# Performance work log

Hardware: AMD Instinct MI355X
Metric: run time of the kernel (lower is better)

## Reference

```python
import jax, jax.numpy as jnp
import numpy as np

H = 8  # num_attention_heads
DH = 64  # attention_head_size
D = H * DH  # hidden_size = 512
LN_EPS = 1e-6


def setup_inputs() -> dict:
    key = jax.random.key(0)
    ks = jax.random.split(key, 12)
    B, L = 32, 196
    s = 1.0 / np.sqrt(D)
    return {
        "query_states": jax.random.normal(ks[0], (B, L, D), jnp.float32),
        "key_states": jax.random.normal(ks[1], (B, L, D), jnp.float32),
        "value_states": jax.random.normal(ks[2], (B, L, D), jnp.float32),
        "Wq": jax.random.normal(ks[3], (D, D), jnp.float32) * s,
        "bq": jnp.zeros((D,), jnp.float32),
        "Wk": jax.random.normal(ks[4], (D, D), jnp.float32) * s,
        "bk": jnp.zeros((D,), jnp.float32),
        "Wv": jax.random.normal(ks[5], (D, D), jnp.float32) * s,
        "bv": jnp.zeros((D,), jnp.float32),
        "ln_gamma": jnp.ones((D,), jnp.float32),
        "ln_beta": jnp.zeros((D,), jnp.float32),
        "logit_scale": jnp.ones((), jnp.float32),
    }


def _heads(x):
    # (B, L, D) -> (B, H, L, DH)
    B, L, _ = x.shape
    return x.reshape(B, L, H, DH).transpose(0, 2, 1, 3)


def reference(query_states, key_states, value_states, Wq, bq, Wk, bk, Wv, bv,
              ln_gamma, ln_beta, logit_scale):
    B, L, _ = query_states.shape
    q = _heads(query_states @ Wq.T + bq)  # (B,H,L,DH)
    k = _heads(key_states @ Wk.T + bk)
    v = _heads(value_states @ Wv.T + bv)

    # cross-batch retrieval: sum over heads and head_dim -> (a,b,l,m)
    retrieve = jnp.einsum('ahld,bhmd->ablm', q, k)
    mask_sum = jnp.float32(L)  # mask is all-ones (B, L)
    t2v = retrieve.max(axis=-1).sum(axis=2) / mask_sum  # (a,b)
    v2t = retrieve.max(axis=-2).sum(axis=2) / mask_sum  # (a,b)
    retrieve_logits = jnp.exp(logit_scale) * (t2v + v2t) / 2.0

    # self-attention (dropout is identity in eval)
    scores = jnp.einsum('bhld,bhmd->bhlm', q, k) / jnp.sqrt(jnp.float32(DH))
    probs = jax.nn.softmax(scores, axis=-1)  # (B,H,L,L)
    ctx = jnp.einsum('bhlm,bhmd->bhld', probs, v)
    ctx = ctx.transpose(0, 2, 1, 3).reshape(B, L, D)
    ctx = ctx + query_states

    mu = ctx.mean(axis=-1, keepdims=True)
    var = ((ctx - mu) ** 2).mean(axis=-1, keepdims=True)
    ctx = (ctx - mu) / jnp.sqrt(var + LN_EPS) * ln_gamma + ln_beta

    return ctx, retrieve_logits, probs.mean(axis=1)
```

## Files before the change

kernel.cpp:

```cpp
#include <hip/hip_runtime.h>
#include <hip/hip_bf16.h>

#define BB 32
#define LL 196
#define DD 512
#define HH 8
#define DHH 64
#define BL (BB*LL)
#define PVK 224
#define PSTR 236

typedef __bf16 bf16x8 __attribute__((ext_vector_type(8)));
typedef float f32x4 __attribute__((ext_vector_type(4)));

#define MFMA16(a,b,c) __builtin_amdgcn_mfma_f32_16x16x32_bf16((a),(b),(c),0,0,0)

#define GLOAD_LDS16(g, l) __builtin_amdgcn_global_load_lds( \
    (const __attribute__((address_space(1))) void*)(g), \
    (__attribute__((address_space(3))) void*)(l), 16, 0, 0)

static __device__ __forceinline__ bf16x8 pack8(float4 v0, float4 v1) {
  bf16x8 o;
  o[0] = (__bf16)v0.x; o[1] = (__bf16)v0.y; o[2] = (__bf16)v0.z; o[3] = (__bf16)v0.w;
  o[4] = (__bf16)v1.x; o[5] = (__bf16)v1.y; o[6] = (__bf16)v1.z; o[7] = (__bf16)v1.w;
  return o;
}

static __device__ __forceinline__ unsigned fkey(float f) {
  unsigned u = __float_as_uint(f);
  return u ^ ((unsigned)((int)u >> 31) | 0x80000000u);
}
static __device__ __forceinline__ float unkey(unsigned k) {
  unsigned u = (k & 0x80000000u) ? (k ^ 0x80000000u) : ~k;
  return __uint_as_float(u);
}

#define STAGE_PAIR(SA, SB, abase, bbase) do { \
  const __bf16* aB_ = (abase); const __bf16* bB_ = (bbase); \
  _Pragma("unroll") \
  for (int c_ = 0; c_ < 4; ++c_) { \
    const int p_ = c_ * 256 + tid; \
    GLOAD_LDS16(aB_ + (size_t)(p_ >> 3) * DD + swoff, &SA[p_ * 8]); \
  } \
  _Pragma("unroll") \
  for (int c_ = 0; c_ < 4; ++c_) { \
    const int p_ = c_ * 256 + tid; \
    GLOAD_LDS16(bB_ + (size_t)(p_ >> 3) * DD + swoff, &SB[p_ * 8]); \
  } \
} while (0)

#define COMPUTE_TILE(SA, SB) do { \
  _Pragma("unroll") \
  for (int kc_ = 0; kc_ < 2; ++kc_) { \
    const int q_ = (((kc_ * 4 + (lane >> 4)) ^ (lane & 7)) << 3); \
    bf16x8 af_[4], bf_[4]; \
    _Pragma("unroll") \
    for (int mt_ = 0; mt_ < 4; ++mt_) \
      af_[mt_] = *(const bf16x8*)&SA[(wr + mt_ * 16 + (lane & 15)) * 64 + q_]; \
    _Pragma("unroll") \
    for (int nt_ = 0; nt_ < 4; ++nt_) \
      bf_[nt_] = *(const bf16x8*)&SB[(wc + nt_ * 16 + (lane & 15)) * 64 + q_]; \
    _Pragma("unroll") \
    for (int mt_ = 0; mt_ < 4; ++mt_) \
      _Pragma("unroll") \
      for (int nt_ = 0; nt_ < 4; ++nt_) \
        acc[mt_][nt_] = MFMA16(af_[mt_], bf_[nt_], acc[mt_][nt_]); \
  } \
} while (0)

__global__ __launch_bounds__(256) void cvt_kernel(
    const float* __restrict__ x0, const float* __restrict__ x1, const float* __restrict__ x2,
    const float* __restrict__ w0, const float* __restrict__ w1, const float* __restrict__ w2,
    __bf16* __restrict__ xb, __bf16* __restrict__ wb)
{
  const int z = blockIdx.y;
  const float* src; __bf16* dst; size_t i;
  if (blockIdx.x < 1568) {
    src = (z == 0) ? x0 : (z == 1) ? x1 : x2;
    dst = xb + (size_t)z * 3211264;
    i = (size_t)blockIdx.x * 256 + threadIdx.x;
  } else {
    src = (z == 0) ? w0 : (z == 1) ? w1 : w2;
    dst = wb + (size_t)z * 262144;
    i = (size_t)(blockIdx.x - 1568) * 256 + threadIdx.x;
  }
  const float4* s = (const float4*)(src + i * 8);
  float4 a = s[0], b = s[1];
  *(bf16x8*)(dst + i * 8) = pack8(a, b);
}

__global__ __launch_bounds__(256) void proj_gemm_kernel(
    const __bf16* __restrict__ xb, const __bf16* __restrict__ wb,
    const float* __restrict__ bq, const float* __restrict__ bk, const float* __restrict__ bv,
    __bf16* __restrict__ qp, __bf16* __restrict__ kp, __bf16* __restrict__ vp)
{
  __shared__ __bf16 sA[128 * 64];
  __shared__ __bf16 sB[128 * 64];

  const int z = blockIdx.z;
  const __bf16* A = xb + (size_t)z * 3211264;
  const __bf16* B = wb + (size_t)z * 262144;
  const float* bias = (z == 0) ? bq : (z == 1) ? bk : bv;
  __bf16* out = (z == 0) ? qp : (z == 1) ? kp : vp;

  const int tid = threadIdx.x;
  const int w = tid >> 6, lane = tid & 63;
  const int wr = (w >> 1) * 64, wc = (w & 1) * 64;
  const int bm = blockIdx.x * 128, bn = blockIdx.y * 128;
  const int swoff = ((tid & 7) ^ ((tid >> 3) & 7)) << 3;

  const __bf16* aP = A + (size_t)bm * DD;
  const __bf16* bP = B + (size_t)bn * DD;

  f32x4 acc[4][4] = {};

  #pragma unroll
  for (int kt = 0; kt < 8; ++kt) {
    STAGE_PAIR(sA, sB, aP + kt * 64, bP + kt * 64);
    __syncthreads();
    COMPUTE_TILE(sA, sB);
    __syncthreads();
  }

  #pragma unroll
  for (int mt = 0; mt < 4; ++mt)
    #pragma unroll
    for (int nt = 0; nt < 4; ++nt)
      #pragma unroll
      for (int rr = 0; rr < 4; ++rr) {
        const int row = bm + wr + mt * 16 + (lane >> 4) * 4 + rr;
        const int col = bn + wc + nt * 16 + (lane & 15);
        out[(size_t)row * DD + col] = (__bf16)(acc[mt][nt][rr] + bias[col]);
      }
}

__global__ __launch_bounds__(256) void transpose_v_kernel(
    const __bf16* __restrict__ vp, __bf16* __restrict__ vpT)
{
  __shared__ __bf16 sT[64][72];
  const int bbh = blockIdx.x;
  const int mt = blockIdx.y;
  const int bb = bbh >> 3, h = bbh & 7;
  const int tid = threadIdx.x;
  {
    const int r = tid >> 2, c0 = (tid & 3) * 16;
    const int m = mt * 64 + r;
    bf16x8 z = {};
    bf16x8 v0 = z, v1 = z;
    if (m < LL) {
      const bf16x8* src = (const bf16x8*)&vp[(size_t)(bb * LL + m) * DD + h * DHH + c0];
      v0 = src[0]; v1 = src[1];
    }
    *(bf16x8*)&sT[r][c0]     = v0;
    *(bf16x8*)&sT[r][c0 + 8] = v1;
  }
  __syncthreads();
  {
    const int d = tid >> 2, mc0 = (tid & 3) * 16;
    if (mt * 64 + mc0 < PVK) {
      bf16x8 o0, o1;
      #pragma unroll
      for (int j = 0; j < 8; ++j) { o0[j] = sT[mc0 + j][d]; o1[j] = sT[mc0 + 8 + j][d]; }
      __bf16* dst = vpT + (size_t)(bbh * 64 + d) * PVK + mt * 64 + mc0;
      *(bf16x8*)dst = o0;
      *(bf16x8*)(dst + 8) = o1;
    }
  }
}

__global__ __launch_bounds__(256) void retrieve_kernel(
    const __bf16* __restrict__ qp, const __bf16* __restrict__ kp,
    unsigned* __restrict__ rmax, unsigned* __restrict__ cmax)
{
  __shared__ __bf16 sA[128 * 64];
  __shared__ __bf16 sB[128 * 64];

  const int orig = blockIdx.x;
  const int xcd = orig & 7, idx = orig >> 3;
  const int wg = (xcd == 0) ? idx : (301 + (xcd - 1) * 300 + idx);
  const int st = wg / 49, wi = wg % 49;
  const int brow = ((st / 7) * 7 + wi / 7) * 128;
  const int bcol = ((st % 7) * 7 + wi % 7) * 128;

  const int tid = threadIdx.x;
  const int w = tid >> 6, lane = tid & 63;
  const int wr = (w >> 1) * 64, wc = (w & 1) * 64;
  const int swoff = ((tid & 7) ^ ((tid >> 3) & 7)) << 3;

  const __bf16* aP = qp + (size_t)brow * DD;
  const __bf16* bP = kp + (size_t)bcol * DD;

  f32x4 acc[4][4] = {};

  #pragma unroll
  for (int kt = 0; kt < 8; ++kt) {
    STAGE_PAIR(sA, sB, aP + kt * 64, bP + kt * 64);
    __syncthreads();
    COMPUTE_TILE(sA, sB);
    __syncthreads();
  }

  const int wcol0 = bcol + wc;
  const int wrow0 = brow + wr;
  {
    const int b0 = wcol0 / LL, b1 = (wcol0 + 63) / LL;
    for (int b = b0; b <= b1; ++b) {
      const int lo = b * LL, hi = lo + LL;
      #pragma unroll
      for (int mt = 0; mt < 4; ++mt)
        #pragma unroll
        for (int rr = 0; rr < 4; ++rr) {
          float m = -3e38f;
          #pragma unroll
          for (int nt = 0; nt < 4; ++nt) {
            const int col = wcol0 + nt * 16 + (lane & 15);
            if (col >= lo && col < hi) m = fmaxf(m, acc[mt][nt][rr]);
          }
          m = fmaxf(m, __shfl_xor(m, 1));
          m = fmaxf(m, __shfl_xor(m, 2));
          m = fmaxf(m, __shfl_xor(m, 4));
          m = fmaxf(m, __shfl_xor(m, 8));
          if ((lane & 15) == 0) {
            const int grow = wrow0 + mt * 16 + (lane >> 4) * 4 + rr;
            atomicMax(&rmax[(size_t)b * BL + grow], fkey(m));
          }
        }
    }
  }
  {
    const int a0 = wrow0 / LL, a1 = (wrow0 + 63) / LL;
    for (int a = a0; a <= a1; ++a) {
      const int lo = a * LL, hi = lo + LL;
      #pragma unroll
      for (int nt = 0; nt < 4; ++nt) {
        float cm = -3e38f;
        #pragma unroll
        for (int mt = 0; mt < 4; ++mt)
          #pragma unroll
          for (int rr = 0; rr < 4; ++rr) {
            const int grow = wrow0 + mt * 16 + (lane >> 4) * 4 + rr;
            if (grow >= lo && grow < hi) cm = fmaxf(cm, acc[mt][nt][rr]);
          }
        cm = fmaxf(cm, __shfl_xor(cm, 16));
        cm = fmaxf(cm, __shfl_xor(cm, 32));
        if (lane < 16) {
          const int col = wcol0 + nt * 16 + lane;
          atomicMax(&cmax[(size_t)a * BL + col], fkey(cm));
        }
      }
    }
  }
}

__global__ __launch_bounds__(256) void finish_kernel(
    const unsigned* __restrict__ rmax, const unsigned* __restrict__ cmax,
    const float* __restrict__ ls, float* __restrict__ out_logits)
{
  const int tid = threadIdx.x;
  const int w = tid >> 6, lane = tid & 63;
  const int pair = blockIdx.x * 4 + w;
  const int a = pair >> 5, b = pair & 31;
  float s = 0.f;
  #pragma unroll
  for (int k = 0; k < 4; ++k) {
    const int l = lane + k * 64;
    if (l < LL) {
      s += unkey(rmax[(size_t)b * BL + a * LL + l]);
      s += unkey(cmax[(size_t)a * BL + b * LL + l]);
    }
  }
  #pragma unroll
  for (int o = 1; o < 64; o <<= 1) s += __shfl_xor(s, o);
  if (lane == 0)
    out_logits[a * BB + b] = expf(ls[0]) * s * (0.5f / (float)LL);
}

__global__ __launch_bounds__(512) void attn_kernel(
    const __bf16* __restrict__ qp, const __bf16* __restrict__ kp,
    const __bf16* __restrict__ vpT, float* __restrict__ ctx,
    float* __restrict__ probs_out)
{
  __shared__ __bf16 pr[8][16][PSTR];

  const int bb = blockIdx.x;
  const int strip = blockIdx.y;
  const int tid = threadIdx.x;
  const int w = tid >> 6, lane = tid & 63;
  const int h = w;
  const int row0 = strip * 16;

  for (int i = lane; i < 256; i += 64)
    pr[w][i >> 4][208 + (i & 15)] = (__bf16)0.f;

  const int arow = row0 + (lane & 15);
  const bool aval = arow < LL;

  bf16x8 aq[2];
  #pragma unroll
  for (int kc = 0; kc < 2; ++kc) {
    bf16x8 z = {};
    aq[kc] = aval
      ? *(const bf16x8*)&qp[(size_t)(bb * LL + arow) * DD + h * DHH + kc * 32 + (lane >> 4) * 8]
      : z;
  }
  f32x4 s[13] = {};
  __builtin_amdgcn_s_setprio(1);
  #pragma unroll
  for (int nt = 0; nt < 13; ++nt) {
    const int brow = nt * 16 + (lane & 15);
    #pragma unroll
    for (int kc = 0; kc < 2; ++kc) {
      bf16x8 bk = {};
      if (brow < LL)
        bk = *(const bf16x8*)&kp[(size_t)(bb * LL + brow) * DD + h * DHH + kc * 32 + (lane >> 4) * 8];
      s[nt] = MFMA16(aq[kc], bk, s[nt]);
    }
  }
  __builtin_amdgcn_s_setprio(0);

  const int colbase = lane & 15;
  #pragma unroll
  for (int nt = 0; nt < 13; ++nt) {
    const bool cv = (nt * 16 + colbase) < LL;
    #pragma unroll
    for (int rr = 0; rr < 4; ++rr)
      s[nt][rr] = cv ? s[nt][rr] * 0.125f : -1e30f;
  }
  float mx[4], dn[4];
  #pragma unroll
  for (int rr = 0; rr < 4; ++rr) {
    float m = s[0][rr];
    #pragma unroll
    for (int nt = 1; nt < 13; ++nt) m = fmaxf(m, s[nt][rr]);
    m = fmaxf(m, __shfl_xor(m, 1));
    m = fmaxf(m, __shfl_xor(m, 2));
    m = fmaxf(m, __shfl_xor(m, 4));
    m = fmaxf(m, __shfl_xor(m, 8));
    mx[rr] = m;
  }
  #pragma unroll
  for (int nt = 0; nt < 13; ++nt)
    #pragma unroll
    for (int rr = 0; rr < 4; ++rr)
      s[nt][rr] = __expf(s[nt][rr] - mx[rr]);
  #pragma unroll
  for (int rr = 0; rr < 4; ++rr) {
    float d = 0.f;
    #pragma unroll
    for (int nt = 0; nt < 13; ++nt) d += s[nt][rr];
    d += __shfl_xor(d, 1);
    d += __shfl_xor(d, 2);
    d += __shfl_xor(d, 4);
    d += __shfl_xor(d, 8);
    dn[rr] = 1.f / d;
  }
  #pragma unroll
  for (int nt = 0; nt < 13; ++nt)
    #pragma unroll
    for (int rr = 0; rr < 4; ++rr)
      pr[w][(lane >> 4) * 4 + rr][nt * 16 + colbase] = (__bf16)(s[nt][rr] * dn[rr]);
  __syncthreads();

  f32x4 c4[4] = {};
  __builtin_amdgcn_s_setprio(1);
  #pragma unroll
  for (int kc = 0; kc < 7; ++kc) {
    bf16x8 ap = *(const bf16x8*)&pr[w][lane & 15][kc * 32 + (lane >> 4) * 8];
    #pragma unroll
    for (int dt = 0; dt < 4; ++dt) {
      bf16x8 bv = *(const bf16x8*)&vpT[(size_t)((bb * 8 + h) * 64 + dt * 16 + (lane & 15)) * PVK + kc * 32 + (lane >> 4) * 8];
      c4[dt] = MFMA16(ap, bv, c4[dt]);
    }
  }
  __builtin_amdgcn_s_setprio(0);
  #pragma unroll
  for (int dt = 0; dt < 4; ++dt)
    #pragma unroll
    for (int rr = 0; rr < 4; ++rr) {
      const int qrow = row0 + (lane >> 4) * 4 + rr;
      if (qrow < LL)
        ctx[(size_t)(bb * LL + qrow) * DD + h * DHH + dt * 16 + (lane & 15)] = c4[dt][rr];
    }

  {
    const int rr_ = tid >> 5;
    const int c0_ = (tid & 31) * 7;
    const int qrow = row0 + rr_;
    if (qrow < LL) {
      #pragma unroll
      for (int j = 0; j < 7; ++j) {
        const int c = c0_ + j;
        if (c < LL) {
          float sum = 0.f;
          #pragma unroll
          for (int ww = 0; ww < 8; ++ww) sum += (float)pr[ww][rr_][c];
          probs_out[((size_t)bb * LL + qrow) * LL + c] = sum * 0.125f;
        }
      }
    }
  }
}

__global__ __launch_bounds__(256) void ln_kernel(
    float* __restrict__ ctx, const float* __restrict__ resid,
    const float* __restrict__ gamma, const float* __restrict__ beta)
{
  const int tid = threadIdx.x;
  const int w = tid >> 6, lane = tid & 63;
  const int row = blockIdx.x * 4 + w;
  float* crow = ctx + (size_t)row * DD;
  const float* rrow = resid + (size_t)row * DD;
  const int c = lane * 8;

  float4 a0 = *(const float4*)(crow + c);
  float4 a1 = *(const float4*)(crow + c + 4);
  float4 b0 = *(const float4*)(rrow + c);
  float4 b1 = *(const float4*)(rrow + c + 4);
  float v[8] = {a0.x + b0.x, a0.y + b0.y, a0.z + b0.z, a0.w + b0.w,
                a1.x + b1.x, a1.y + b1.y, a1.z + b1.z, a1.w + b1.w};

  float sum = 0.f;
  #pragma unroll
  for (int j = 0; j < 8; ++j) sum += v[j];
  #pragma unroll
  for (int o = 1; o < 64; o <<= 1) sum += __shfl_xor(sum, o);
  const float mu = sum * (1.f / (float)DD);

  float var = 0.f;
  #pragma unroll
  for (int j = 0; j < 8; ++j) { float d = v[j] - mu; var += d * d; }
  #pragma unroll
  for (int o = 1; o < 64; o <<= 1) var += __shfl_xor(var, o);
  const float rstd = rsqrtf(var * (1.f / (float)DD) + 1e-6f);

  float4 g0 = *(const float4*)(gamma + c);
  float4 g1 = *(const float4*)(gamma + c + 4);
  float4 e0 = *(const float4*)(beta + c);
  float4 e1 = *(const float4*)(beta + c + 4);
  float g[8] = {g0.x, g0.y, g0.z, g0.w, g1.x, g1.y, g1.z, g1.w};
  float e[8] = {e0.x, e0.y, e0.z, e0.w, e1.x, e1.y, e1.z, e1.w};

  float o_[8];
  #pragma unroll
  for (int j = 0; j < 8; ++j) o_[j] = (v[j] - mu) * rstd * g[j] + e[j];
  *(float4*)(crow + c)     = make_float4(o_[0], o_[1], o_[2], o_[3]);
  *(float4*)(crow + c + 4) = make_float4(o_[4], o_[5], o_[6], o_[7]);
}

extern "C" void kernel_launch(void* const* d_in, const int* in_sizes, int n_in,
                              void* d_out, int out_size, void* d_ws, size_t ws_size,
                              hipStream_t stream)
{
  const float* xq    = (const float*)d_in[0];
  const float* xk    = (const float*)d_in[1];
  const float* xv    = (const float*)d_in[2];
  const float* Wq    = (const float*)d_in[3];
  const float* bq    = (const float*)d_in[4];
  const float* Wk    = (const float*)d_in[5];
  const float* bk    = (const float*)d_in[6];
  const float* Wv    = (const float*)d_in[7];
  const float* bv    = (const float*)d_in[8];
  const float* gamma = (const float*)d_in[9];
  const float* beta  = (const float*)d_in[10];
  const float* ls    = (const float*)d_in[11];

  float* out_ctx    = (float*)d_out;
  float* out_logits = out_ctx + (size_t)BL * DD;
  float* out_probs  = out_logits + BB * BB;

  const size_t xsz = (size_t)BL * DD;
  const size_t wsz = (size_t)DD * DD;
  __bf16* xb = (__bf16*)d_ws;
  __bf16* wb = xb + 3 * xsz;
  __bf16* qp = wb + 3 * wsz;
  __bf16* kp = qp + xsz;
  __bf16* vp = kp + xsz;
  __bf16* vpT = xb;
  unsigned* rmax = (unsigned*)(xb + 3670016);
  unsigned* cmax = rmax + (size_t)BB * BL;

  cvt_kernel<<<dim3(1696, 3), 256, 0, stream>>>(xq, xk, xv, Wq, Wk, Wv, xb, wb);

  proj_gemm_kernel<<<dim3(49, 4, 3), 256, 0, stream>>>(xb, wb, bq, bk, bv, qp, kp, vp);

  transpose_v_kernel<<<dim3(BB * HH, 4), 256, 0, stream>>>(vp, vpT);

  hipMemsetAsync(rmax, 0, (size_t)2 * BB * BL * sizeof(unsigned), stream);

  retrieve_kernel<<<2401, 256, 0, stream>>>(qp, kp, rmax, cmax);
  finish_kernel<<<256, 256, 0, stream>>>(rmax, cmax, ls, out_logits);

  attn_kernel<<<dim3(BB, 13), 512, 0, stream>>>(qp, kp, vpT, out_ctx, out_probs);
  ln_kernel<<<BL / 4, 256, 0, stream>>>(out_ctx, xq, gamma, beta);
}
```

Before: 237.7 us.

## Retile retrieve GEMM to 256x256 blocks with 4-stage async LDS pipeline

Reworks the cross-batch retrieve GEMM from 128x128 tiles with 256 threads to 256x256 tiles with 512 threads (8 waves, each 128x64), using a 4-deep ring of k=32 LDS stages loaded via global_load_lds with explicit vmcnt waits and s_setprio around the MFMA bursts. Q/K buffers are padded to 6400 rows and the pad is zeroed, so tiles need no bounds checks during loads; the atomics are guarded instead. The aim is to raise arithmetic intensity per byte loaded and overlap loads with MFMA. The cost is 128KB of LDS and two extra memsets, and the larger grid tiles leave the final row and column of tiles mostly padding.

```diff
diff --git a/kernel.cpp b/kernel.cpp
--- a/kernel.cpp
+++ b/kernel.cpp
@@ -7,6 +7,7 @@
 #define HH 8
 #define DHH 64
 #define BL (BB*LL)
+#define NPAD 6400
 #define PVK 224
 #define PSTR 236
 
@@ -33,6 +34,27 @@
 static __device__ __forceinline__ float unkey(unsigned k) {
   unsigned u = (k & 0x80000000u) ? (k ^ 0x80000000u) : ~k;
   return __uint_as_float(u);
+}
+
+__global__ __launch_bounds__(256) void cvt_kernel(
+    const float* __restrict__ x0, const float* __restrict__ x1, const float* __restrict__ x2,
+    const float* __restrict__ w0, const float* __restrict__ w1, const float* __restrict__ w2,
+    __bf16* __restrict__ xb, __bf16* __restrict__ wb)
+{
+  const int z = blockIdx.y;
+  const float* src; __bf16* dst; size_t i;
+  if (blockIdx.x < 1568) {
+    src = (z == 0) ? x0 : (z == 1) ? x1 : x2;
+    dst = xb + (size_t)z * 3211264;
+    i = (size_t)blockIdx.x * 256 + threadIdx.x;
+  } else {
+    src = (z == 0) ? w0 : (z == 1) ? w1 : w2;
+    dst = wb + (size_t)z * 262144;
+    i = (size_t)(blockIdx.x - 1568) * 256 + threadIdx.x;
+  }
+  const float4* s = (const float4*)(src + i * 8);
+  float4 a = s[0], b = s[1];
+  *(bf16x8*)(dst + i * 8) = pack8(a, b);
 }
 
 #define STAGE_PAIR(SA, SB, abase, bbase) do { \
@@ -68,27 +90,6 @@
   } \
 } while (0)
 
-__global__ __launch_bounds__(256) void cvt_kernel(
-    const float* __restrict__ x0, const float* __restrict__ x1, const float* __restrict__ x2,
-    const float* __restrict__ w0, const float* __restrict__ w1, const float* __restrict__ w2,
-    __bf16* __restrict__ xb, __bf16* __restrict__ wb)
-{
-  const int z = blockIdx.y;
-  const float* src; __bf16* dst; size_t i;
-  if (blockIdx.x < 1568) {
-    src = (z == 0) ? x0 : (z == 1) ? x1 : x2;
-    dst = xb + (size_t)z * 3211264;
-    i = (size_t)blockIdx.x * 256 + threadIdx.x;
-  } else {
-    src = (z == 0) ? w0 : (z == 1) ? w1 : w2;
-    dst = wb + (size_t)z * 262144;
-    i = (size_t)(blockIdx.x - 1568) * 256 + threadIdx.x;
-  }
-  const float4* s = (const float4*)(src + i * 8);
-  float4 a = s[0], b = s[1];
-  *(bf16x8*)(dst + i * 8) = pack8(a, b);
-}
-
 __global__ __launch_bounds__(256) void proj_gemm_kernel(
     const __bf16* __restrict__ xb, const __bf16* __restrict__ wb,
     const float* __restrict__ bq, const float* __restrict__ bk, const float* __restrict__ bv,
@@ -168,46 +169,81 @@
   }
 }
 
-__global__ __launch_bounds__(256) void retrieve_kernel(
+#define STAGE_T(T) do { \
+  char* la_ = ldsb + ((T) & 3) * 32768; \
+  const __bf16* ga_ = aG + (T) * 32; \
+  const __bf16* gb_ = bG + (T) * 32; \
+  GLOAD_LDS16(ga_,            la_ + tid * 16); \
+  GLOAD_LDS16(ga_ + 128 * DD, la_ + 8192 + tid * 16); \
+  GLOAD_LDS16(gb_,            la_ + 16384 + tid * 16); \
+  GLOAD_LDS16(gb_ + 128 * DD, la_ + 24576 + tid * 16); \
+} while (0)
+
+#define RITER(T, VM) do { \
+  if ((T) + 3 < 16) { STAGE_T((T) + 3); } \
+  asm volatile("s_waitcnt vmcnt(" #VM ")" ::: "memory"); \
+  __builtin_amdgcn_s_barrier(); \
+  { \
+    const __bf16* lA_ = (const __bf16*)(ldsb + ((T) & 3) * 32768); \
+    const __bf16* lB_ = lA_ + 8192; \
+    bf16x8 bfr_[4]; \
+    _Pragma("unroll") \
+    for (int nt_ = 0; nt_ < 4; ++nt_) \
+      bfr_[nt_] = *(const bf16x8*)&lB_[(wc + nt_ * 16 + (lane & 15)) * 32 + rswz]; \
+    __builtin_amdgcn_s_setprio(1); \
+    _Pragma("unroll") \
+    for (int mt_ = 0; mt_ < 8; ++mt_) { \
+      bf16x8 af_ = *(const bf16x8*)&lA_[(wr + mt_ * 16 + (lane & 15)) * 32 + rswz]; \
+      _Pragma("unroll") \
+      for (int nt_ = 0; nt_ < 4; ++nt_) \
+        acc[mt_][nt_] = MFMA16(af_, bfr_[nt_], acc[mt_][nt_]); \
+    } \
+    __builtin_amdgcn_s_setprio(0); \
+  } \
+  __builtin_amdgcn_s_barrier(); \
+} while (0)
+
+__global__ __launch_bounds__(512, 2) void retrieve_kernel(
     const __bf16* __restrict__ qp, const __bf16* __restrict__ kp,
     unsigned* __restrict__ rmax, unsigned* __restrict__ cmax)
 {
-  __shared__ __bf16 sA[128 * 64];
-  __shared__ __bf16 sB[128 * 64];
+  __shared__ char ldsb[131072];
 
   const int orig = blockIdx.x;
   const int xcd = orig & 7, idx = orig >> 3;
-  const int wg = (xcd == 0) ? idx : (301 + (xcd - 1) * 300 + idx);
-  const int st = wg / 49, wi = wg % 49;
-  const int brow = ((st / 7) * 7 + wi / 7) * 128;
-  const int bcol = ((st % 7) * 7 + wi % 7) * 128;
+  const int wg = (xcd == 0) ? idx : (79 + (xcd - 1) * 78 + idx);
+  const int st = wg / 25, wi = wg % 25;
+  const int brow = ((st / 5) * 5 + wi / 5) * 256;
+  const int bcol = ((st % 5) * 5 + wi % 5) * 256;
 
   const int tid = threadIdx.x;
-  const int w = tid >> 6, lane = tid & 63;
-  const int wr = (w >> 1) * 64, wc = (w & 1) * 64;
-  const int swoff = ((tid & 7) ^ ((tid >> 3) & 7)) << 3;
-
-  const __bf16* aP = qp + (size_t)brow * DD;
-  const __bf16* bP = kp + (size_t)bcol * DD;
-
-  f32x4 acc[4][4] = {};
-
-  #pragma unroll
-  for (int kt = 0; kt < 8; ++kt) {
-    STAGE_PAIR(sA, sB, aP + kt * 64, bP + kt * 64);
-    __syncthreads();
-    COMPUTE_TILE(sA, sB);
-    __syncthreads();
-  }
+  const int wid = tid >> 6, lane = tid & 63;
+  const int wr = (wid >> 2) * 128, wc = (wid & 3) * 64;
+
+  const int sswz = (tid & 3) ^ ((tid >> 2) & 3) ^ ((tid >> 4) & 3);
+  const __bf16* aG = qp + (size_t)(brow + (tid >> 2)) * DD + sswz * 8;
+  const __bf16* bG = kp + (size_t)(bcol + (tid >> 2)) * DD + sswz * 8;
+
+  const int rswz = ((lane >> 4) ^ (lane & 3) ^ ((lane >> 2) & 3)) << 3;
+
+  f32x4 acc[8][4] = {};
+
+  STAGE_T(0); STAGE_T(1); STAGE_T(2);
+
+  RITER(0, 12);  RITER(1, 12);  RITER(2, 12);  RITER(3, 12);
+  RITER(4, 12);  RITER(5, 12);  RITER(6, 12);  RITER(7, 12);
+  RITER(8, 12);  RITER(9, 12);  RITER(10, 12); RITER(11, 12);
+  RITER(12, 12); RITER(13, 8);  RITER(14, 4);  RITER(15, 0);
 
   const int wcol0 = bcol + wc;
   const int wrow0 = brow + wr;
   {
-    const int b0 = wcol0 / LL, b1 = (wcol0 + 63) / LL;
-    for (int b = b0; b <= b1; ++b) {
+    const int b0 = wcol0 / LL;
+    const int b1 = (wcol0 + 63) / LL;
+    for (int b = b0; b <= b1 && b < BB; ++b) {
       const int lo = b * LL, hi = lo + LL;
       #pragma unroll
-      for (int mt = 0; mt < 4; ++mt)
+      for (int mt = 0; mt < 8; ++mt)
         #pragma unroll
         for (int rr = 0; rr < 4; ++rr) {
           float m = -3e38f;
@@ -222,20 +258,21 @@
           m = fmaxf(m, __shfl_xor(m, 8));
           if ((lane & 15) == 0) {
             const int grow = wrow0 + mt * 16 + (lane >> 4) * 4 + rr;
-            atomicMax(&rmax[(size_t)b * BL + grow], fkey(m));
+            if (grow < BL) atomicMax(&rmax[(size_t)b * BL + grow], fkey(m));
           }
         }
     }
   }
   {
-    const int a0 = wrow0 / LL, a1 = (wrow0 + 63) / LL;
-    for (int a = a0; a <= a1; ++a) {
+    const int a0 = wrow0 / LL;
+    const int a1 = (wrow0 + 127) / LL;
+    for (int a = a0; a <= a1 && a < BB; ++a) {
       const int lo = a * LL, hi = lo + LL;
       #pragma unroll
       for (int nt = 0; nt < 4; ++nt) {
         float cm = -3e38f;
         #pragma unroll
-        for (int mt = 0; mt < 4; ++mt)
+        for (int mt = 0; mt < 8; ++mt)
           #pragma unroll
           for (int rr = 0; rr < 4; ++rr) {
             const int grow = wrow0 + mt * 16 + (lane >> 4) * 4 + rr;
@@ -245,7 +282,7 @@
         cm = fmaxf(cm, __shfl_xor(cm, 32));
         if (lane < 16) {
           const int col = wcol0 + nt * 16 + lane;
-          atomicMax(&cmax[(size_t)a * BL + col], fkey(cm));
+          if (col < BL) atomicMax(&cmax[(size_t)a * BL + col], fkey(cm));
         }
       }
     }
@@ -470,11 +507,12 @@
 
   const size_t xsz = (size_t)BL * DD;
   const size_t wsz = (size_t)DD * DD;
+  const size_t qsz = (size_t)NPAD * DD;
   __bf16* xb = (__bf16*)d_ws;
   __bf16* wb = xb + 3 * xsz;
   __bf16* qp = wb + 3 * wsz;
-  __bf16* kp = qp + xsz;
-  __bf16* vp = kp + xsz;
+  __bf16* kp = qp + qsz;
+  __bf16* vp = kp + qsz;
   __bf16* vpT = xb;
   unsigned* rmax = (unsigned*)(xb + 3670016);
   unsigned* cmax = rmax + (size_t)BB * BL;
@@ -485,9 +523,11 @@
 
   transpose_v_kernel<<<dim3(BB * HH, 4), 256, 0, stream>>>(vp, vpT);
 
+  hipMemsetAsync(qp + (size_t)BL * DD, 0, (size_t)(NPAD - BL) * DD * sizeof(__bf16), stream);
+  hipMemsetAsync(kp + (size_t)BL * DD, 0, (size_t)(NPAD - BL) * DD * sizeof(__bf16), stream);
   hipMemsetAsync(rmax, 0, (size_t)2 * BB * BL * sizeof(unsigned), stream);
 
-  retrieve_kernel<<<2401, 256, 0, stream>>>(qp, kp, rmax, cmax);
+  retrieve_kernel<<<625, 512, 0, stream>>>(qp, kp, rmax, cmax);
   finish_kernel<<<256, 256, 0, stream>>>(rmax, cmax, ls, out_logits);
 
   attn_kernel<<<dim3(BB, 13), 512, 0, stream>>>(qp, kp, vpT, out_ctx, out_probs);
```

Result: slower. 260.0 us (+9.4%).
